# Performance work log

Measured on AMD Instinct MI355X. Metric: run time of the kernel, lower is better.

Reference implementation:

```python
import jax, jax.numpy as jnp
import numpy as np

N_DOMAIN = 8
EPS = 1e-5
N, F = 262144, 512


def setup_inputs() -> dict:
    key = jax.random.key(0)
    k1, k2, k3, k4 = jax.random.split(key, 4)
    x = jax.random.normal(k1, (N, F), dtype=jnp.float32)
    y = jax.random.randint(k2, (N,), 0, N_DOMAIN)  # domain id per row
    # per-domain affine params of each BatchNorm1d (randomized for non-trivial grads)
    gamma = jax.random.uniform(k3, (N_DOMAIN, F), dtype=jnp.float32, minval=0.5, maxval=1.5)
    beta = 0.1 * jax.random.normal(k4, (N_DOMAIN, F), dtype=jnp.float32)
    return {"x": x, "y": y, "gamma": gamma, "beta": beta}


def reference(x, y, gamma, beta):
    # Fused domain-specific BatchNorm: per-domain batch mean/var via segmented
    # reductions, then normalize each row with its domain's stats.
    ones = jnp.ones((x.shape[0],), dtype=x.dtype)
    counts = jax.ops.segment_sum(ones, y, num_segments=N_DOMAIN)          # [D]
    sums = jax.ops.segment_sum(x, y, num_segments=N_DOMAIN)               # [D, F]
    sumsq = jax.ops.segment_sum(x * x, y, num_segments=N_DOMAIN)          # [D, F]
    safe = jnp.maximum(counts, 1.0)[:, None]
    mean = sums / safe                                                     # [D, F]
    var = sumsq / safe - mean * mean                                       # biased var (BN training)
    # count==1: torch code flips to eval mode -> uses running stats (fresh: mean=0, var=1)
    use_batch = (counts > 1.0)[:, None]
    mean_e = jnp.where(use_batch, mean, 0.0)
    var_e = jnp.where(use_batch, var, 1.0)
    inv = jax.lax.rsqrt(var_e + EPS)                                       # [D, F]
    out = gamma[y] * (x - mean_e[y]) * inv[y] + beta[y]                    # [N, F]
    # count==0 rows stay zero (out buffer initialized to zeros in torch code)
    out = jnp.where((counts[y] > 0.0)[:, None], out, 0.0)
    return out
```

## Files before the change

kernel.cpp:

```cpp
#include <hip/hip_runtime.h>

#define N_ROWS 262144
#define NF 512
#define ND 8
#define F4 128
#define EPSV 1e-5f

#define G1 256
#define B1 512
#define ROWS_PER_B1 (N_ROWS / G1)
#define PSTRIDE 8448
#define NG2 16

#define G3 1024
#define B3 512
#define ROWS_PER_B3 (N_ROWS / G3)

#define ACC1(D, V)                                              \
    sum[D][0] += (V).x; sq[D][0] = fmaf((V).x, (V).x, sq[D][0]); \
    sum[D][1] += (V).y; sq[D][1] = fmaf((V).y, (V).y, sq[D][1]); \
    sum[D][2] += (V).z; sq[D][2] = fmaf((V).z, (V).z, sq[D][2]); \
    sum[D][3] += (V).w; sq[D][3] = fmaf((V).w, (V).w, sq[D][3]); \
    cnt[D] += cinc;

#define ACCUM(DD, V) switch (DD) {            \
    case 0: { ACC1(0, V) } break;             \
    case 1: { ACC1(1, V) } break;             \
    case 2: { ACC1(2, V) } break;             \
    case 3: { ACC1(3, V) } break;             \
    case 4: { ACC1(4, V) } break;             \
    case 5: { ACC1(5, V) } break;             \
    case 6: { ACC1(6, V) } break;             \
    default: { ACC1(7, V) } break; }

__global__ __launch_bounds__(B1, 2) void k1_partial(
    const float* __restrict__ x, const int* __restrict__ y,
    float* __restrict__ part ) {
  __shared__ float sSum[4][ND][F4];
  __shared__ float sSq[4][ND][F4];
  __shared__ float sCnt[ND];

  float sum[ND][4];
  float sq[ND][4];
  float cnt[ND];
#pragma unroll
  for (int d = 0; d < ND; ++d) {
    cnt[d] = 0.0f;
#pragma unroll
    for (int j = 0; j < 4; ++j) { sum[d][j] = 0.0f; sq[d][j] = 0.0f; }
  }

  const int tid = threadIdx.x;
  const int f4 = tid & (F4 - 1);
  const int rg = tid >> 7;
  const float cinc = (f4 == 0) ? 1.0f : 0.0f;
  const float4* __restrict__ x4 = (const float4*)x;
  const int rowBase = blockIdx.x * ROWS_PER_B1;

  for (int r0 = 0; r0 < ROWS_PER_B1; r0 += 16) {
    const int r = rowBase + r0 + rg;
    float4 v0 = x4[(size_t)(r +  0) * F4 + f4];
    float4 v1 = x4[(size_t)(r +  4) * F4 + f4];
    float4 v2 = x4[(size_t)(r +  8) * F4 + f4];
    float4 v3 = x4[(size_t)(r + 12) * F4 + f4];
    const int d0 = __builtin_amdgcn_readfirstlane(y[r +  0]);
    const int d1 = __builtin_amdgcn_readfirstlane(y[r +  4]);
    const int d2 = __builtin_amdgcn_readfirstlane(y[r +  8]);
    const int d3 = __builtin_amdgcn_readfirstlane(y[r + 12]);
    ACCUM(d0, v0)
    ACCUM(d1, v1)
    ACCUM(d2, v2)
    ACCUM(d3, v3)
  }

  for (int p = 0; p < 4; ++p) {
    if (rg == p) {
#pragma unroll
      for (int d = 0; d < ND; ++d) {
#pragma unroll
        for (int j = 0; j < 4; ++j) {
          if (p == 0) { sSum[j][d][f4] = sum[d][j]; sSq[j][d][f4] = sq[d][j]; }
          else        { sSum[j][d][f4] += sum[d][j]; sSq[j][d][f4] += sq[d][j]; }
        }
        if (f4 == 0) {
          if (p == 0) sCnt[d] = cnt[d]; else sCnt[d] += cnt[d];
        }
      }
    }
    __syncthreads();
  }

  float* __restrict__ pb = part + (size_t)blockIdx.x * PSTRIDE;
  for (int i = tid; i < 8200; i += B1) {
    float v;
    if (i < 4096) {
      const int d = i >> 9, f = i & 511;
      v = sSum[f & 3][d][f >> 2];
    } else if (i < 8192) {
      const int k = i - 4096;
      const int d = k >> 9, f = k & 511;
      v = sSq[f & 3][d][f >> 2];
    } else {
      v = sCnt[i - 8192];
    }
    pb[i] = v;
  }
}

__global__ void k1b_reduce(const float* __restrict__ part, float* __restrict__ p2) {
  const int i = blockIdx.x * 256 + threadIdx.x;
  if (i >= 8200) return;
  const int c = blockIdx.y;
  const float* __restrict__ p = part + (size_t)c * 16 * PSTRIDE + i;
  float a0 = 0.f, a1 = 0.f, a2 = 0.f, a3 = 0.f;
#pragma unroll
  for (int g = 0; g < 16; g += 4) {
    a0 += p[(size_t)(g + 0) * PSTRIDE];
    a1 += p[(size_t)(g + 1) * PSTRIDE];
    a2 += p[(size_t)(g + 2) * PSTRIDE];
    a3 += p[(size_t)(g + 3) * PSTRIDE];
  }
  p2[(size_t)c * PSTRIDE + i] = (a0 + a1) + (a2 + a3);
}

__global__ void k2_finalize(const float* __restrict__ p2,
                            const float* __restrict__ gamma,
                            const float* __restrict__ beta,
                            float* __restrict__ ss ) {
  const int i = blockIdx.x * 256 + threadIdx.x;
  const int d = i >> 9;
  float s = 0.f, q = 0.f, c = 0.f;
#pragma unroll
  for (int cc = 0; cc < NG2; ++cc) {
    const float* __restrict__ p = p2 + (size_t)cc * PSTRIDE;
    s += p[i];
    q += p[4096 + i];
    c += p[8192 + d];
  }
  const float safe = fmaxf(c, 1.0f);
  const float mean = s / safe;
  const float var = q / safe - mean * mean;
  const bool ub = c > 1.0f;
  const float mean_e = ub ? mean : 0.0f;
  const float var_e = ub ? var : 1.0f;
  const float inv = rsqrtf(var_e + EPSV);
  float scale = gamma[i] * inv;
  float shift = beta[i] - scale * mean_e;
  if (!(c > 0.0f)) { scale = 0.0f; shift = 0.0f; }
  ss[i] = scale;
  ss[4096 + i] = shift;
}

__global__ __launch_bounds__(B3) void k3_normalize(
    const float* __restrict__ x, const int* __restrict__ y,
    const float* __restrict__ ss, float* __restrict__ out) {
  const int tid = threadIdx.x;
  const int f4 = tid & (F4 - 1);
  const int rg = tid >> 7;
  const float4* __restrict__ x4 = (const float4*)x;
  const float4* __restrict__ s4 = (const float4*)ss;
  const float4* __restrict__ t4 = (const float4*)(ss + 4096);
  float4* __restrict__ o4 = (float4*)out;
  const int rowBase = blockIdx.x * ROWS_PER_B3;

  for (int r0 = 0; r0 < ROWS_PER_B3; r0 += 8) {
    const int ra = rowBase + r0 + rg;
    const int rb = ra + 4;
    float4 va = x4[(size_t)ra * F4 + f4];
    float4 vb = x4[(size_t)rb * F4 + f4];
    const int da = y[ra];
    const int db = y[rb];
    float4 sa = s4[da * F4 + f4];
    float4 ta = t4[da * F4 + f4];
    float4 sb = s4[db * F4 + f4];
    float4 tb = t4[db * F4 + f4];
    float4 oa, ob;
    oa.x = fmaf(sa.x, va.x, ta.x);
    oa.y = fmaf(sa.y, va.y, ta.y);
    oa.z = fmaf(sa.z, va.z, ta.z);
    oa.w = fmaf(sa.w, va.w, ta.w);
    ob.x = fmaf(sb.x, vb.x, tb.x);
    ob.y = fmaf(sb.y, vb.y, tb.y);
    ob.z = fmaf(sb.z, vb.z, tb.z);
    ob.w = fmaf(sb.w, vb.w, tb.w);
    o4[(size_t)ra * F4 + f4] = oa;
    o4[(size_t)rb * F4 + f4] = ob;
  }
}

extern "C" void kernel_launch(void* const* d_in, const int* in_sizes, int n_in,
                              void* d_out, int out_size, void* d_ws, size_t ws_size,
                              hipStream_t stream) {
  const float* x     = (const float*)d_in[0];
  const int*   y     = (const int*)d_in[1];
  const float* gamma = (const float*)d_in[2];
  const float* beta  = (const float*)d_in[3];
  float* out = (float*)d_out;
  float* ws  = (float*)d_ws;

  float* p1 = out;
  float* p2 = out + (size_t)G1 * PSTRIDE;

  k1_partial<<<G1, B1, 0, stream>>>(x, y, p1);
  k1b_reduce<<<dim3(33, NG2), 256, 0, stream>>>(p1, p2);
  k2_finalize<<<16, 256, 0, stream>>>(p2, gamma, beta, ws);
  k3_normalize<<<G3, B3, 0, stream>>>(x, y, ws, out);
}
```

Baseline: 1.001 ms.

## Stage scale/shift and labels in LDS, drop reduce pass, use nontemporal stores

```diff
diff --git a/kernel.cpp b/kernel.cpp
--- a/kernel.cpp
+++ b/kernel.cpp
@@ -10,11 +10,18 @@
 #define B1 512
 #define ROWS_PER_B1 (N_ROWS / G1)
 #define PSTRIDE 8448
-#define NG2 16
 
 #define G3 1024
 #define B3 512
 #define ROWS_PER_B3 (N_ROWS / G3)
+
+typedef float f32x4 __attribute__((ext_vector_type(4)));
+
+static __device__ __forceinline__ void nt_store4(float4 v, float4* p) {
+  f32x4 w;
+  w.x = v.x; w.y = v.y; w.z = v.z; w.w = v.w;
+  __builtin_nontemporal_store(w, (f32x4*)p);
+}
 
 #define ACC1(D, V)                                              \
     sum[D][0] += (V).x; sq[D][0] = fmaf((V).x, (V).x, sq[D][0]); \
@@ -39,6 +46,7 @@
   __shared__ float sSum[4][ND][F4];
   __shared__ float sSq[4][ND][F4];
   __shared__ float sCnt[ND];
+  __shared__ int sY[ROWS_PER_B1];
 
   float sum[ND][4];
   float sq[ND][4];
@@ -57,16 +65,20 @@
   const float4* __restrict__ x4 = (const float4*)x;
   const int rowBase = blockIdx.x * ROWS_PER_B1;
 
+  for (int i = tid; i < ROWS_PER_B1; i += B1) sY[i] = y[rowBase + i];
+  __syncthreads();
+
   for (int r0 = 0; r0 < ROWS_PER_B1; r0 += 16) {
-    const int r = rowBase + r0 + rg;
+    const int lr = r0 + rg;
+    const int r = rowBase + lr;
     float4 v0 = x4[(size_t)(r +  0) * F4 + f4];
     float4 v1 = x4[(size_t)(r +  4) * F4 + f4];
     float4 v2 = x4[(size_t)(r +  8) * F4 + f4];
     float4 v3 = x4[(size_t)(r + 12) * F4 + f4];
-    const int d0 = __builtin_amdgcn_readfirstlane(y[r +  0]);
-    const int d1 = __builtin_amdgcn_readfirstlane(y[r +  4]);
-    const int d2 = __builtin_amdgcn_readfirstlane(y[r +  8]);
-    const int d3 = __builtin_amdgcn_readfirstlane(y[r + 12]);
+    const int d0 = __builtin_amdgcn_readfirstlane(sY[lr +  0]);
+    const int d1 = __builtin_amdgcn_readfirstlane(sY[lr +  4]);
+    const int d2 = __builtin_amdgcn_readfirstlane(sY[lr +  8]);
+    const int d3 = __builtin_amdgcn_readfirstlane(sY[lr + 12]);
     ACCUM(d0, v0)
     ACCUM(d1, v1)
     ACCUM(d2, v2)
@@ -107,36 +119,28 @@
   }
 }
 
-__global__ void k1b_reduce(const float* __restrict__ part, float* __restrict__ p2) {
-  const int i = blockIdx.x * 256 + threadIdx.x;
-  if (i >= 8200) return;
-  const int c = blockIdx.y;
-  const float* __restrict__ p = part + (size_t)c * 16 * PSTRIDE + i;
-  float a0 = 0.f, a1 = 0.f, a2 = 0.f, a3 = 0.f;
-#pragma unroll
-  for (int g = 0; g < 16; g += 4) {
-    a0 += p[(size_t)(g + 0) * PSTRIDE];
-    a1 += p[(size_t)(g + 1) * PSTRIDE];
-    a2 += p[(size_t)(g + 2) * PSTRIDE];
-    a3 += p[(size_t)(g + 3) * PSTRIDE];
-  }
-  p2[(size_t)c * PSTRIDE + i] = (a0 + a1) + (a2 + a3);
-}
-
-__global__ void k2_finalize(const float* __restrict__ p2,
+__global__ void k2_finalize(const float* __restrict__ part,
                             const float* __restrict__ gamma,
                             const float* __restrict__ beta,
                             float* __restrict__ ss ) {
-  const int i = blockIdx.x * 256 + threadIdx.x;
+  const int i = blockIdx.x * 128 + threadIdx.x;
   const int d = i >> 9;
-  float s = 0.f, q = 0.f, c = 0.f;
-#pragma unroll
-  for (int cc = 0; cc < NG2; ++cc) {
-    const float* __restrict__ p = p2 + (size_t)cc * PSTRIDE;
-    s += p[i];
-    q += p[4096 + i];
-    c += p[8192 + d];
-  }
+  float sa[4] = {0.f, 0.f, 0.f, 0.f};
+  float qa[4] = {0.f, 0.f, 0.f, 0.f};
+  float ca[4] = {0.f, 0.f, 0.f, 0.f};
+  for (int b = 0; b < G1; b += 4) {
+#pragma unroll
+    for (int u = 0; u < 4; ++u) {
+      const float* __restrict__ p = part + (size_t)(b + u) * PSTRIDE;
+      sa[u] += p[i];
+      qa[u] += p[4096 + i];
+      ca[u] += p[8192 + d];
+    }
+  }
+  const float s = (sa[0] + sa[1]) + (sa[2] + sa[3]);
+  const float q = (qa[0] + qa[1]) + (qa[2] + qa[3]);
+  const float c = (ca[0] + ca[1]) + (ca[2] + ca[3]);
+
   const float safe = fmaxf(c, 1.0f);
   const float mean = s / safe;
   const float var = q / safe - mean * mean;
@@ -151,40 +155,57 @@
   ss[4096 + i] = shift;
 }
 
-__global__ __launch_bounds__(B3) void k3_normalize(
+__global__ __launch_bounds__(B3, 2) void k3_normalize(
     const float* __restrict__ x, const int* __restrict__ y,
     const float* __restrict__ ss, float* __restrict__ out) {
+  __shared__ float4 sS[ND * F4];
+  __shared__ float4 sT[ND * F4];
+  __shared__ int sy[ROWS_PER_B3];
+
   const int tid = threadIdx.x;
+  const int rowBase = (G3 - 1 - (int)blockIdx.x) * ROWS_PER_B3;
+
+  const float4* __restrict__ ssv = (const float4*)ss;
+  sS[tid]       = ssv[tid];
+  sS[tid + 512] = ssv[tid + 512];
+  sT[tid]       = ssv[1024 + tid];
+  sT[tid + 512] = ssv[1536 + tid];
+  if (tid < ROWS_PER_B3) sy[tid] = y[rowBase + tid];
+  __syncthreads();
+
   const int f4 = tid & (F4 - 1);
   const int rg = tid >> 7;
   const float4* __restrict__ x4 = (const float4*)x;
-  const float4* __restrict__ s4 = (const float4*)ss;
-  const float4* __restrict__ t4 = (const float4*)(ss + 4096);
   float4* __restrict__ o4 = (float4*)out;
-  const int rowBase = blockIdx.x * ROWS_PER_B3;
-
-  for (int r0 = 0; r0 < ROWS_PER_B3; r0 += 8) {
-    const int ra = rowBase + r0 + rg;
-    const int rb = ra + 4;
-    float4 va = x4[(size_t)ra * F4 + f4];
-    float4 vb = x4[(size_t)rb * F4 + f4];
-    const int da = y[ra];
-    const int db = y[rb];
-    float4 sa = s4[da * F4 + f4];
-    float4 ta = t4[da * F4 + f4];
-    float4 sb = s4[db * F4 + f4];
-    float4 tb = t4[db * F4 + f4];
-    float4 oa, ob;
-    oa.x = fmaf(sa.x, va.x, ta.x);
-    oa.y = fmaf(sa.y, va.y, ta.y);
-    oa.z = fmaf(sa.z, va.z, ta.z);
-    oa.w = fmaf(sa.w, va.w, ta.w);
-    ob.x = fmaf(sb.x, vb.x, tb.x);
-    ob.y = fmaf(sb.y, vb.y, tb.y);
-    ob.z = fmaf(sb.z, vb.z, tb.z);
-    ob.w = fmaf(sb.w, vb.w, tb.w);
-    o4[(size_t)ra * F4 + f4] = oa;
-    o4[(size_t)rb * F4 + f4] = ob;
+
+  for (int r0 = 0; r0 < ROWS_PER_B3; r0 += 16) {
+    const int lr = r0 + rg;
+    const size_t g = (size_t)(rowBase + lr) * F4 + f4;
+    float4 v0 = x4[g];
+    float4 v1 = x4[g +  4 * F4];
+    float4 v2 = x4[g +  8 * F4];
+    float4 v3 = x4[g + 12 * F4];
+    const int d0 = sy[lr];
+    const int d1 = sy[lr + 4];
+    const int d2 = sy[lr + 8];
+    const int d3 = sy[lr + 12];
+    float4 s0 = sS[d0 * F4 + f4], t0 = sT[d0 * F4 + f4];
+    float4 s1 = sS[d1 * F4 + f4], t1 = sT[d1 * F4 + f4];
+    float4 s2 = sS[d2 * F4 + f4], t2 = sT[d2 * F4 + f4];
+    float4 s3 = sS[d3 * F4 + f4], t3 = sT[d3 * F4 + f4];
+    float4 o0, o1, o2, o3;
+    o0.x = fmaf(s0.x, v0.x, t0.x); o0.y = fmaf(s0.y, v0.y, t0.y);
+    o0.z = fmaf(s0.z, v0.z, t0.z); o0.w = fmaf(s0.w, v0.w, t0.w);
+    o1.x = fmaf(s1.x, v1.x, t1.x); o1.y = fmaf(s1.y, v1.y, t1.y);
+    o1.z = fmaf(s1.z, v1.z, t1.z); o1.w = fmaf(s1.w, v1.w, t1.w);
+    o2.x = fmaf(s2.x, v2.x, t2.x); o2.y = fmaf(s2.y, v2.y, t2.y);
+    o2.z = fmaf(s2.z, v2.z, t2.z); o2.w = fmaf(s2.w, v2.w, t2.w);
+    o3.x = fmaf(s3.x, v3.x, t3.x); o3.y = fmaf(s3.y, v3.y, t3.y);
+    o3.z = fmaf(s3.z, v3.z, t3.z); o3.w = fmaf(s3.w, v3.w, t3.w);
+    nt_store4(o0, &o4[g]);
+    nt_store4(o1, &o4[g +  4 * F4]);
+    nt_store4(o2, &o4[g +  8 * F4]);
+    nt_store4(o3, &o4[g + 12 * F4]);
   }
 }
 
@@ -199,10 +220,8 @@
   float* ws  = (float*)d_ws;
 
   float* p1 = out;
-  float* p2 = out + (size_t)G1 * PSTRIDE;
 
   k1_partial<<<G1, B1, 0, stream>>>(x, y, p1);
-  k1b_reduce<<<dim3(33, NG2), 256, 0, stream>>>(p1, p2);
-  k2_finalize<<<16, 256, 0, stream>>>(p2, gamma, beta, ws);
+  k2_finalize<<<32, 128, 0, stream>>>(p1, gamma, beta, ws);
   k3_normalize<<<G3, B3, 0, stream>>>(x, y, ws, out);
 }
```

After: 998.9 us. Within noise of the previous version (-0.2%).
